# Kernel optimization log

Hardware: AMD Instinct MI355X
Metric: run time of the kernel (lower is better)

## Reference

```python
import jax, jax.numpy as jnp
import numpy as np

N_NODES = 50000
N_EDGES = 800000
HIDDEN = 128
N_GRAPHS = 64


def _linear_init(key, fan_in, shape):
    # torch.nn.Linear default init: U(-1/sqrt(fan_in), 1/sqrt(fan_in))
    bound = 1.0 / np.sqrt(fan_in)
    return jax.random.uniform(key, shape, jnp.float32, -bound, bound)


def setup_inputs() -> dict:
    key = jax.random.key(0)
    ks = jax.random.split(key, 13)
    x = jax.random.normal(ks[0], (N_NODES, HIDDEN), jnp.float32)
    edge_index = jax.random.randint(ks[1], (2, N_EDGES), 0, N_NODES, dtype=jnp.int64)
    batch = jnp.sort(jax.random.randint(ks[2], (N_NODES,), 0, N_GRAPHS, dtype=jnp.int64))
    H = HIDDEN
    return {
        "x": x,
        "edge_index": edge_index,
        "batch": batch,
        "W1a": _linear_init(ks[3], H, (H, H)),
        "b1a": _linear_init(ks[4], H, (H,)),
        "W2a": _linear_init(ks[5], H, (H, H)),
        "b2a": _linear_init(ks[6], H, (H,)),
        "W1b": _linear_init(ks[7], H, (H, H)),
        "b1b": _linear_init(ks[8], H, (H,)),
        "W2b": _linear_init(ks[9], H, (H, H)),
        "b2b": _linear_init(ks[10], H, (H,)),
        "Wfc": _linear_init(ks[11], H, (H, 1)),
        "bfc": _linear_init(ks[12], H, (1,)),
    }


def _gin_conv(x, src, dst, W1, b1, W2, b2):
    # GINConv with eps=0: mlp((1+eps)*x + sum_{j->i} x_j)
    agg = jax.ops.segment_sum(x[src], dst, num_segments=N_NODES) + x
    h = jax.nn.gelu(agg @ W1 + b1, approximate=False)  # exact erf GELU (torch default)
    return jax.nn.gelu(h @ W2 + b2, approximate=False)


def reference(x, edge_index, batch, W1a, b1a, W2a, b2a, W1b, b1b, W2b, b2b, Wfc, bfc):
    src, dst = edge_index[0], edge_index[1]  # messages flow src -> dst (PyG convention)
    h = _gin_conv(x, src, dst, W1a, b1a, W2a, b2a)
    h = _gin_conv(h, src, dst, W1b, b1b, W2b, b2b)
    y = h @ Wfc + bfc  # [N, 1]
    return jax.ops.segment_sum(y, batch, num_segments=N_GRAPHS)  # [G, 1]
```

## Files before the change

### kernel.cpp

```cpp
#include <hip/hip_runtime.h>
#include <hip/hip_bf16.h>
#include <math.h>

#define N_NODES 50000
#define N_EDGES 800000
#define HID 128
#define N_GRAPHS 64
#define BCAP 64

#define ELOOP 8
#define EB ((N_EDGES + 256 * ELOOP - 1) / (256 * ELOOP))
#define RANGES 8
#define RSPAN ((N_NODES + RANGES - 1) / RANGES)
#define CONV_B 782
#define PREP_B 256
#define PREP_GRID (EB * RANGES + CONV_B + PREP_B)

typedef __bf16 bfv8 __attribute__((ext_vector_type(8)));
typedef float f32x4 __attribute__((ext_vector_type(4)));

__device__ __forceinline__ unsigned short f2bf(float f) {
    unsigned int u = __float_as_uint(f);
    u += 0x7fff + ((u >> 16) & 1);
    return (unsigned short)(u >> 16);
}
__device__ __forceinline__ float bflo(unsigned int u) { return __uint_as_float(u << 16); }
__device__ __forceinline__ float bfhi(unsigned int u) { return __uint_as_float(u & 0xffff0000u); }

__device__ __forceinline__ float gelu_f(float x) {
    float x3 = x * x * x;
    float z = 1.5957691216f * x + 0.0713548162f * x3;
    float e = __expf(z);
    float t = 1.f - 2.f / (e + 1.f);
    return 0.5f * x * (1.f + t);
}

__global__ __launch_bounds__(256) void prep_all(
    const int* __restrict__ src, const int* __restrict__ dst,
    int* __restrict__ counts, unsigned short* __restrict__ bucket,
    const float4* __restrict__ xin, ushort4* __restrict__ xb4,
    const float* __restrict__ W1a, const float* __restrict__ W2a,
    const float* __restrict__ W1b, const float* __restrict__ W2b,
    unsigned short* __restrict__ Wt) {
    int b = blockIdx.x;
    int t = threadIdx.x;
    if (b < EB * RANGES) {
        int r = b % RANGES;
        int chunk = b / RANGES;
        int lo = r * RSPAN;
        int hi = min(lo + RSPAN, N_NODES);
        int e0 = chunk * (256 * ELOOP) + t;
        #pragma unroll
        for (int j = 0; j < ELOOP; ++j) {
            int e = e0 + j * 256;
            if (e < N_EDGES) {
                int d = dst[e];
                if (d >= lo && d < hi) {
                    int pos = atomicAdd(&counts[d], 1);
                    if (pos < BCAP) bucket[(size_t)d * BCAP + pos] = (unsigned short)src[e];
                }
            }
        }
    } else if (b < EB * RANGES + CONV_B) {
        int bc = b - EB * RANGES;
        const int n4 = N_NODES * HID / 4;
        #pragma unroll
        for (int j = 0; j < 8; ++j) {
            int i = bc * 2048 + j * 256 + t;
            if (i < n4) {
                float4 v = xin[i];
                ushort4 o;
                o.x = f2bf(v.x); o.y = f2bf(v.y); o.z = f2bf(v.z); o.w = f2bf(v.w);
                xb4[i] = o;
            }
        }
    } else {
        int i = (b - EB * RANGES - CONV_B) * 256 + t;
        int m = i >> 14;
        int rr = (i >> 7) & 127;
        int cc = i & 127;
        const float* W = (m == 0) ? W1a : (m == 1) ? W2a : (m == 2) ? W1b : W2b;
        Wt[i] = f2bf(W[cc * HID + rr]);
    }
}

__global__ __launch_bounds__(256) void aggregate8(const unsigned short* __restrict__ xb,
                                                  const int* __restrict__ counts,
                                                  const unsigned short* __restrict__ bucket,
                                                  unsigned short* __restrict__ agg) {
    int node = blockIdx.x * 4 + (threadIdx.x >> 6);
    if (node >= N_NODES) return;
    int lane = threadIdx.x & 63;
    int g = lane >> 3;
    int c = lane & 7;
    int cnt = min(counts[node], BCAP);
    int eidx = (int)bucket[(size_t)node * BCAP + lane];
    float a[16];
    #pragma unroll
    for (int j = 0; j < 16; ++j) a[j] = 0.f;
    int kmax = (cnt + 7) >> 3;
    #pragma unroll 2
    for (int k = 0; k < kmax; ++k) {
        int i = 8 * k + g;
        int s = __shfl(eidx, (i < cnt) ? i : 0);
        if (i < cnt) {
            const unsigned short* row = xb + (size_t)s * HID + c * 16;
            uint4 u0 = *(const uint4*)(row);
            uint4 u1 = *(const uint4*)(row + 8);
            a[0] += bflo(u0.x); a[1] += bfhi(u0.x);
            a[2] += bflo(u0.y); a[3] += bfhi(u0.y);
            a[4] += bflo(u0.z); a[5] += bfhi(u0.z);
            a[6] += bflo(u0.w); a[7] += bfhi(u0.w);
            a[8] += bflo(u1.x); a[9] += bfhi(u1.x);
            a[10] += bflo(u1.y); a[11] += bfhi(u1.y);
            a[12] += bflo(u1.z); a[13] += bfhi(u1.z);
            a[14] += bflo(u1.w); a[15] += bfhi(u1.w);
        }
    }
    #pragma unroll
    for (int j = 0; j < 16; ++j) {
        a[j] += __shfl_xor(a[j], 8);
        a[j] += __shfl_xor(a[j], 16);
        a[j] += __shfl_xor(a[j], 32);
    }
    if (g == 0) {
        const unsigned short* row = xb + (size_t)node * HID + c * 16;
        uint4 u0 = *(const uint4*)(row);
        uint4 u1 = *(const uint4*)(row + 8);
        a[0] += bflo(u0.x); a[1] += bfhi(u0.x);
        a[2] += bflo(u0.y); a[3] += bfhi(u0.y);
        a[4] += bflo(u0.z); a[5] += bfhi(u0.z);
        a[6] += bflo(u0.w); a[7] += bfhi(u0.w);
        a[8] += bflo(u1.x); a[9] += bfhi(u1.x);
        a[10] += bflo(u1.y); a[11] += bfhi(u1.y);
        a[12] += bflo(u1.z); a[13] += bfhi(u1.z);
        a[14] += bflo(u1.w); a[15] += bfhi(u1.w);
        uint4 o0, o1;
        o0.x = (unsigned int)f2bf(a[0]) | ((unsigned int)f2bf(a[1]) << 16);
        o0.y = (unsigned int)f2bf(a[2]) | ((unsigned int)f2bf(a[3]) << 16);
        o0.z = (unsigned int)f2bf(a[4]) | ((unsigned int)f2bf(a[5]) << 16);
        o0.w = (unsigned int)f2bf(a[6]) | ((unsigned int)f2bf(a[7]) << 16);
        o1.x = (unsigned int)f2bf(a[8]) | ((unsigned int)f2bf(a[9]) << 16);
        o1.y = (unsigned int)f2bf(a[10]) | ((unsigned int)f2bf(a[11]) << 16);
        o1.z = (unsigned int)f2bf(a[12]) | ((unsigned int)f2bf(a[13]) << 16);
        o1.w = (unsigned int)f2bf(a[14]) | ((unsigned int)f2bf(a[15]) << 16);
        unsigned short* orow = agg + (size_t)node * HID + c * 16;
        *(uint4*)(orow) = o0;
        *(uint4*)(orow + 8) = o1;
    }
}

#define LDP 136
__global__ __launch_bounds__(512) void mlp_fused(const unsigned short* __restrict__ A,
                                                 const unsigned short* __restrict__ Wt1,
                                                 const float* __restrict__ b1,
                                                 const unsigned short* __restrict__ Wt2,
                                                 const float* __restrict__ b2,
                                                 unsigned short* __restrict__ out, int nrows) {
    __shared__ __align__(16) unsigned short sA[128][LDP];
    __shared__ __align__(16) unsigned short sT[128][LDP];
    const int t = threadIdx.x;
    const int row0 = blockIdx.x * 128;

    #pragma unroll
    for (int rr = 0; rr < 4; ++rr) {
        int idx = t + rr * 512;
        int r = idx >> 4;
        int cb = (idx & 15) * 8;
        int gr = row0 + r;
        ulonglong2 v = {0ull, 0ull};
        if (gr < nrows) v = *(const ulonglong2*)(A + (size_t)gr * HID + cb);
        *(ulonglong2*)(&sA[r][cb]) = v;
    }

    const int w = t >> 6;
    const int l = t & 63;
    const int lr = l & 15;
    const int lkg = l >> 4;
    const int lk = lkg * 8;
    const int cw = w * 16 + lr;

    bfv8 w1f[4], w2f[4];
    #pragma unroll
    for (int kc = 0; kc < 4; ++kc) {
        w1f[kc] = *(const bfv8*)(Wt1 + (size_t)cw * HID + kc * 32 + lk);
        w2f[kc] = *(const bfv8*)(Wt2 + (size_t)cw * HID + kc * 32 + lk);
    }
    float bias1 = b1[cw];
    float bias2 = b2[cw];
    __syncthreads();

    f32x4 acc[8];
    #pragma unroll
    for (int m = 0; m < 8; ++m) acc[m] = (f32x4){0.f, 0.f, 0.f, 0.f};
    #pragma unroll
    for (int m = 0; m < 8; ++m) {
        #pragma unroll
        for (int kc = 0; kc < 4; ++kc) {
            bfv8 af = *(const bfv8*)(&sA[m * 16 + lr][kc * 32 + lk]);
            acc[m] = __builtin_amdgcn_mfma_f32_16x16x32_bf16(af, w1f[kc], acc[m], 0, 0, 0);
        }
    }
    #pragma unroll
    for (int m = 0; m < 8; ++m) {
        #pragma unroll
        for (int i = 0; i < 4; ++i) {
            float v = gelu_f(acc[m][i] + bias1);
            sT[m * 16 + lkg * 4 + i][cw] = f2bf(v);
        }
    }
    __syncthreads();

    #pragma unroll
    for (int m = 0; m < 8; ++m) acc[m] = (f32x4){0.f, 0.f, 0.f, 0.f};
    #pragma unroll
    for (int m = 0; m < 8; ++m) {
        #pragma unroll
        for (int kc = 0; kc < 4; ++kc) {
            bfv8 af = *(const bfv8*)(&sT[m * 16 + lr][kc * 32 + lk]);
            acc[m] = __builtin_amdgcn_mfma_f32_16x16x32_bf16(af, w2f[kc], acc[m], 0, 0, 0);
        }
    }
    #pragma unroll
    for (int m = 0; m < 8; ++m) {
        #pragma unroll
        for (int i = 0; i < 4; ++i) {
            float v = gelu_f(acc[m][i] + bias2);
            sA[m * 16 + lkg * 4 + i][cw] = f2bf(v);
        }
    }
    __syncthreads();
    #pragma unroll
    for (int rr = 0; rr < 4; ++rr) {
        int idx = t + rr * 512;
        int r = idx >> 4;
        int cb = (idx & 15) * 8;
        int gr = row0 + r;
        if (gr < nrows)
            *(ulonglong2*)(out + (size_t)gr * HID + cb) = *(const ulonglong2*)(&sA[r][cb]);
    }
}

__global__ __launch_bounds__(512) void mlp_final(const unsigned short* __restrict__ A,
                                                 const unsigned short* __restrict__ Wt1,
                                                 const float* __restrict__ b1,
                                                 const unsigned short* __restrict__ Wt2,
                                                 const float* __restrict__ b2,
                                                 const float* __restrict__ Wfc,
                                                 const float* __restrict__ bfc,
                                                 const int* __restrict__ batch,
                                                 float* __restrict__ out, int nrows) {
    __shared__ __align__(16) unsigned short sA[128][LDP];
    __shared__ __align__(16) unsigned short sT[128][LDP];
    __shared__ float bins[N_GRAPHS];
    const int t = threadIdx.x;
    const int row0 = blockIdx.x * 128;
    if (t < N_GRAPHS) bins[t] = 0.f;

    #pragma unroll
    for (int rr = 0; rr < 4; ++rr) {
        int idx = t + rr * 512;
        int r = idx >> 4;
        int cb = (idx & 15) * 8;
        int gr = row0 + r;
        ulonglong2 v = {0ull, 0ull};
        if (gr < nrows) v = *(const ulonglong2*)(A + (size_t)gr * HID + cb);
        *(ulonglong2*)(&sA[r][cb]) = v;
    }

    const int w = t >> 6;
    const int l = t & 63;
    const int lr = l & 15;
    const int lkg = l >> 4;
    const int lk = lkg * 8;
    const int cw = w * 16 + lr;

    bfv8 w1f[4], w2f[4];
    #pragma unroll
    for (int kc = 0; kc < 4; ++kc) {
        w1f[kc] = *(const bfv8*)(Wt1 + (size_t)cw * HID + kc * 32 + lk);
        w2f[kc] = *(const bfv8*)(Wt2 + (size_t)cw * HID + kc * 32 + lk);
    }
    float bias1 = b1[cw];
    float bias2 = b2[cw];
    __syncthreads();

    f32x4 acc[8];
    #pragma unroll
    for (int m = 0; m < 8; ++m) acc[m] = (f32x4){0.f, 0.f, 0.f, 0.f};
    #pragma unroll
    for (int m = 0; m < 8; ++m) {
        #pragma unroll
        for (int kc = 0; kc < 4; ++kc) {
            bfv8 af = *(const bfv8*)(&sA[m * 16 + lr][kc * 32 + lk]);
            acc[m] = __builtin_amdgcn_mfma_f32_16x16x32_bf16(af, w1f[kc], acc[m], 0, 0, 0);
        }
    }
    #pragma unroll
    for (int m = 0; m < 8; ++m) {
        #pragma unroll
        for (int i = 0; i < 4; ++i) {
            float v = gelu_f(acc[m][i] + bias1);
            sT[m * 16 + lkg * 4 + i][cw] = f2bf(v);
        }
    }
    __syncthreads();

    #pragma unroll
    for (int m = 0; m < 8; ++m) acc[m] = (f32x4){0.f, 0.f, 0.f, 0.f};
    #pragma unroll
    for (int m = 0; m < 8; ++m) {
        #pragma unroll
        for (int kc = 0; kc < 4; ++kc) {
            bfv8 af = *(const bfv8*)(&sT[m * 16 + lr][kc * 32 + lk]);
            acc[m] = __builtin_amdgcn_mfma_f32_16x16x32_bf16(af, w2f[kc], acc[m], 0, 0, 0);
        }
    }
    #pragma unroll
    for (int m = 0; m < 8; ++m) {
        #pragma unroll
        for (int i = 0; i < 4; ++i) {
            float v = gelu_f(acc[m][i] + bias2);
            sA[m * 16 + lkg * 4 + i][cw] = f2bf(v);
        }
    }
    __syncthreads();

    {
        int row = w * 16 + (l >> 2);
        int q = l & 3;
        int gr = row0 + row;
        float acc2 = 0.f;
        if (gr < nrows) {
            const uint4* hrow = (const uint4*)(&sA[row][q * 32]);
            #pragma unroll
            for (int jj = 0; jj < 4; ++jj) {
                uint4 v = hrow[jj];
                int f = q * 32 + jj * 8;
                acc2 += bflo(v.x) * Wfc[f]     + bfhi(v.x) * Wfc[f + 1];
                acc2 += bflo(v.y) * Wfc[f + 2] + bfhi(v.y) * Wfc[f + 3];
                acc2 += bflo(v.z) * Wfc[f + 4] + bfhi(v.z) * Wfc[f + 5];
                acc2 += bflo(v.w) * Wfc[f + 6] + bfhi(v.w) * Wfc[f + 7];
            }
        }
        acc2 += __shfl_xor(acc2, 1);
        acc2 += __shfl_xor(acc2, 2);
        if (q == 0 && gr < nrows) atomicAdd(&bins[batch[gr]], acc2 + bfc[0]);
    }
    __syncthreads();
    if (t < N_GRAPHS && bins[t] != 0.f) atomicAdd(&out[t], bins[t]);
}

extern "C" void kernel_launch(void* const* d_in, const int* in_sizes, int n_in,
                              void* d_out, int out_size, void* d_ws, size_t ws_size,
                              hipStream_t stream) {
    const float* x    = (const float*)d_in[0];
    const int*   ei   = (const int*)d_in[1];
    const int*   bat  = (const int*)d_in[2];
    const float* W1a  = (const float*)d_in[3];
    const float* b1a  = (const float*)d_in[4];
    const float* W2a  = (const float*)d_in[5];
    const float* b2a  = (const float*)d_in[6];
    const float* W1b  = (const float*)d_in[7];
    const float* b1b  = (const float*)d_in[8];
    const float* W2b  = (const float*)d_in[9];
    const float* b2b  = (const float*)d_in[10];
    const float* Wfc  = (const float*)d_in[11];
    const float* bfc  = (const float*)d_in[12];
    float* out = (float*)d_out;

    const int* src = ei;
    const int* dst = ei + N_EDGES;

    unsigned short* xb     = (unsigned short*)d_ws;
    unsigned short* bufA   = xb + (size_t)N_NODES * HID;
    unsigned short* bufB   = bufA + (size_t)N_NODES * HID;
    unsigned short* Wt     = bufB + (size_t)N_NODES * HID;
    int* counts = (int*)(Wt + 4 * HID * HID);
    unsigned short* bucket = (unsigned short*)(counts + N_NODES);

    hipMemsetAsync(out, 0, N_GRAPHS * sizeof(float), stream);
    hipMemsetAsync(counts, 0, N_NODES * sizeof(int), stream);

    prep_all<<<PREP_GRID, 256, 0, stream>>>(src, dst, counts, bucket,
                                            (const float4*)x, (ushort4*)xb,
                                            W1a, W2a, W1b, W2b, Wt);

    const int agg_blocks = (N_NODES + 3) / 4;
    const int mlp_blocks = (N_NODES + 127) / 128;
    unsigned short* Wt1a = Wt;
    unsigned short* Wt2a = Wt + HID * HID;
    unsigned short* Wt1b = Wt + 2 * HID * HID;
    unsigned short* Wt2b = Wt + 3 * HID * HID;

    aggregate8<<<agg_blocks, 256, 0, stream>>>(xb, counts, bucket, bufA);
    mlp_fused<<<mlp_blocks, 512, 0, stream>>>(bufA, Wt1a, b1a, Wt2a, b2a, bufB, N_NODES);

    aggregate8<<<agg_blocks, 256, 0, stream>>>(bufB, counts, bucket, bufA);
    mlp_final<<<mlp_blocks, 512, 0, stream>>>(bufA, Wt1b, b1b, Wt2b, b2b,
                                              Wfc, bfc, bat, out, N_NODES);
}
```

Before: 240.0 us.

## Pad edge counters, process two nodes per wave, halve MLP row tile

Edge bucketing drops the eight-way destination-range replication: each edge is now visited once, and its per-node counter is padded to a 64-byte stride to reduce atomic contention on shared cache lines. The aggregation kernel now has each wavefront handle two nodes, interleaving their gathers to expose more memory-level parallelism. Both MLP kernels move from 128-row to 64-row tiles, doubling the block count and halving shared memory per block. The costs are a 16x larger counter array to memset, more registers in the aggregation kernel, and weight fragments reloaded per block twice as often.

```diff
diff --git a/kernel.cpp b/kernel.cpp
--- a/kernel.cpp
+++ b/kernel.cpp
@@ -7,14 +7,13 @@
 #define HID 128
 #define N_GRAPHS 64
 #define BCAP 64
+#define CSTR 16
 
 #define ELOOP 8
 #define EB ((N_EDGES + 256 * ELOOP - 1) / (256 * ELOOP))
-#define RANGES 8
-#define RSPAN ((N_NODES + RANGES - 1) / RANGES)
 #define CONV_B 782
 #define PREP_B 256
-#define PREP_GRID (EB * RANGES + CONV_B + PREP_B)
+#define PREP_GRID (EB + CONV_B + PREP_B)
 
 typedef __bf16 bfv8 __attribute__((ext_vector_type(8)));
 typedef float f32x4 __attribute__((ext_vector_type(4)));
@@ -44,25 +43,19 @@
     unsigned short* __restrict__ Wt) {
     int b = blockIdx.x;
     int t = threadIdx.x;
-    if (b < EB * RANGES) {
-        int r = b % RANGES;
-        int chunk = b / RANGES;
-        int lo = r * RSPAN;
-        int hi = min(lo + RSPAN, N_NODES);
-        int e0 = chunk * (256 * ELOOP) + t;
+    if (b < EB) {
+        int e0 = b * (256 * ELOOP) + t;
         #pragma unroll
         for (int j = 0; j < ELOOP; ++j) {
             int e = e0 + j * 256;
             if (e < N_EDGES) {
                 int d = dst[e];
-                if (d >= lo && d < hi) {
-                    int pos = atomicAdd(&counts[d], 1);
-                    if (pos < BCAP) bucket[(size_t)d * BCAP + pos] = (unsigned short)src[e];
-                }
+                int pos = atomicAdd(&counts[d * CSTR], 1);
+                if (pos < BCAP) bucket[(size_t)d * BCAP + pos] = (unsigned short)src[e];
             }
         }
-    } else if (b < EB * RANGES + CONV_B) {
-        int bc = b - EB * RANGES;
+    } else if (b < EB + CONV_B) {
+        int bc = b - EB;
         const int n4 = N_NODES * HID / 4;
         #pragma unroll
         for (int j = 0; j < 8; ++j) {
@@ -75,7 +68,7 @@
             }
         }
     } else {
-        int i = (b - EB * RANGES - CONV_B) * 256 + t;
+        int i = (b - EB - CONV_B) * 256 + t;
         int m = i >> 14;
         int rr = (i >> 7) & 127;
         int cc = i & 127;
@@ -88,65 +81,113 @@
                                                   const int* __restrict__ counts,
                                                   const unsigned short* __restrict__ bucket,
                                                   unsigned short* __restrict__ agg) {
-    int node = blockIdx.x * 4 + (threadIdx.x >> 6);
-    if (node >= N_NODES) return;
-    int lane = threadIdx.x & 63;
-    int g = lane >> 3;
-    int c = lane & 7;
-    int cnt = min(counts[node], BCAP);
-    int eidx = (int)bucket[(size_t)node * BCAP + lane];
-    float a[16];
-    #pragma unroll
-    for (int j = 0; j < 16; ++j) a[j] = 0.f;
-    int kmax = (cnt + 7) >> 3;
-    #pragma unroll 2
-    for (int k = 0; k < kmax; ++k) {
+    int wid = threadIdx.x >> 6;
+    int node0 = blockIdx.x * 8 + wid * 2;
+    int node1 = node0 + 1;
+    bool v0 = node0 < N_NODES, v1 = node1 < N_NODES;
+    if (!v0) return;
+    int l = threadIdx.x & 63;
+    int g = l >> 3;
+    int c = l & 7;
+    int cnt0 = min(counts[node0 * CSTR], BCAP);
+    int cnt1 = v1 ? min(counts[node1 * CSTR], BCAP) : 0;
+    int e0 = (int)bucket[(size_t)node0 * BCAP + l];
+    int e1 = v1 ? (int)bucket[(size_t)node1 * BCAP + l] : 0;
+    float a0[16], a1[16];
+    #pragma unroll
+    for (int j = 0; j < 16; ++j) { a0[j] = 0.f; a1[j] = 0.f; }
+    int km = max((cnt0 + 7) >> 3, (cnt1 + 7) >> 3);
+    for (int k = 0; k < km; ++k) {
         int i = 8 * k + g;
-        int s = __shfl(eidx, (i < cnt) ? i : 0);
-        if (i < cnt) {
-            const unsigned short* row = xb + (size_t)s * HID + c * 16;
+        int s0 = __shfl(e0, (i < cnt0) ? i : 0);
+        int s1 = __shfl(e1, (i < cnt1) ? i : 0);
+        if (i < cnt0) {
+            const unsigned short* row = xb + (size_t)s0 * HID + c * 16;
             uint4 u0 = *(const uint4*)(row);
             uint4 u1 = *(const uint4*)(row + 8);
-            a[0] += bflo(u0.x); a[1] += bfhi(u0.x);
-            a[2] += bflo(u0.y); a[3] += bfhi(u0.y);
-            a[4] += bflo(u0.z); a[5] += bfhi(u0.z);
-            a[6] += bflo(u0.w); a[7] += bfhi(u0.w);
-            a[8] += bflo(u1.x); a[9] += bfhi(u1.x);
-            a[10] += bflo(u1.y); a[11] += bfhi(u1.y);
-            a[12] += bflo(u1.z); a[13] += bfhi(u1.z);
-            a[14] += bflo(u1.w); a[15] += bfhi(u1.w);
+            a0[0] += bflo(u0.x); a0[1] += bfhi(u0.x);
+            a0[2] += bflo(u0.y); a0[3] += bfhi(u0.y);
+            a0[4] += bflo(u0.z); a0[5] += bfhi(u0.z);
+            a0[6] += bflo(u0.w); a0[7] += bfhi(u0.w);
+            a0[8] += bflo(u1.x); a0[9] += bfhi(u1.x);
+            a0[10] += bflo(u1.y); a0[11] += bfhi(u1.y);
+            a0[12] += bflo(u1.z); a0[13] += bfhi(u1.z);
+            a0[14] += bflo(u1.w); a0[15] += bfhi(u1.w);
+        }
+        if (i < cnt1) {
+            const unsigned short* row = xb + (size_t)s1 * HID + c * 16;
+            uint4 u0 = *(const uint4*)(row);
+            uint4 u1 = *(const uint4*)(row + 8);
+            a1[0] += bflo(u0.x); a1[1] += bfhi(u0.x);
+            a1[2] += bflo(u0.y); a1[3] += bfhi(u0.y);
+            a1[4] += bflo(u0.z); a1[5] += bfhi(u0.z);
+            a1[6] += bflo(u0.w); a1[7] += bfhi(u0.w);
+            a1[8] += bflo(u1.x); a1[9] += bfhi(u1.x);
+            a1[10] += bflo(u1.y); a1[11] += bfhi(u1.y);
+            a1[12] += bflo(u1.z); a1[13] += bfhi(u1.z);
+            a1[14] += bflo(u1.w); a1[15] += bfhi(u1.w);
         }
     }
     #pragma unroll
     for (int j = 0; j < 16; ++j) {
-        a[j] += __shfl_xor(a[j], 8);
-        a[j] += __shfl_xor(a[j], 16);
-        a[j] += __shfl_xor(a[j], 32);
+        a0[j] += __shfl_xor(a0[j], 8);
+        a0[j] += __shfl_xor(a0[j], 16);
+        a0[j] += __shfl_xor(a0[j], 32);
+        a1[j] += __shfl_xor(a1[j], 8);
+        a1[j] += __shfl_xor(a1[j], 16);
+        a1[j] += __shfl_xor(a1[j], 32);
     }
     if (g == 0) {
-        const unsigned short* row = xb + (size_t)node * HID + c * 16;
-        uint4 u0 = *(const uint4*)(row);
-        uint4 u1 = *(const uint4*)(row + 8);
-        a[0] += bflo(u0.x); a[1] += bfhi(u0.x);
-        a[2] += bflo(u0.y); a[3] += bfhi(u0.y);
-        a[4] += bflo(u0.z); a[5] += bfhi(u0.z);
-        a[6] += bflo(u0.w); a[7] += bfhi(u0.w);
-        a[8] += bflo(u1.x); a[9] += bfhi(u1.x);
-        a[10] += bflo(u1.y); a[11] += bfhi(u1.y);
-        a[12] += bflo(u1.z); a[13] += bfhi(u1.z);
-        a[14] += bflo(u1.w); a[15] += bfhi(u1.w);
-        uint4 o0, o1;
-        o0.x = (unsigned int)f2bf(a[0]) | ((unsigned int)f2bf(a[1]) << 16);
-        o0.y = (unsigned int)f2bf(a[2]) | ((unsigned int)f2bf(a[3]) << 16);
-        o0.z = (unsigned int)f2bf(a[4]) | ((unsigned int)f2bf(a[5]) << 16);
-        o0.w = (unsigned int)f2bf(a[6]) | ((unsigned int)f2bf(a[7]) << 16);
-        o1.x = (unsigned int)f2bf(a[8]) | ((unsigned int)f2bf(a[9]) << 16);
-        o1.y = (unsigned int)f2bf(a[10]) | ((unsigned int)f2bf(a[11]) << 16);
-        o1.z = (unsigned int)f2bf(a[12]) | ((unsigned int)f2bf(a[13]) << 16);
-        o1.w = (unsigned int)f2bf(a[14]) | ((unsigned int)f2bf(a[15]) << 16);
-        unsigned short* orow = agg + (size_t)node * HID + c * 16;
-        *(uint4*)(orow) = o0;
-        *(uint4*)(orow + 8) = o1;
+        {
+            const unsigned short* row = xb + (size_t)node0 * HID + c * 16;
+            uint4 u0 = *(const uint4*)(row);
+            uint4 u1 = *(const uint4*)(row + 8);
+            a0[0] += bflo(u0.x); a0[1] += bfhi(u0.x);
+            a0[2] += bflo(u0.y); a0[3] += bfhi(u0.y);
+            a0[4] += bflo(u0.z); a0[5] += bfhi(u0.z);
+            a0[6] += bflo(u0.w); a0[7] += bfhi(u0.w);
+            a0[8] += bflo(u1.x); a0[9] += bfhi(u1.x);
+            a0[10] += bflo(u1.y); a0[11] += bfhi(u1.y);
+            a0[12] += bflo(u1.z); a0[13] += bfhi(u1.z);
+            a0[14] += bflo(u1.w); a0[15] += bfhi(u1.w);
+            uint4 o0, o1;
+            o0.x = (unsigned int)f2bf(a0[0]) | ((unsigned int)f2bf(a0[1]) << 16);
+            o0.y = (unsigned int)f2bf(a0[2]) | ((unsigned int)f2bf(a0[3]) << 16);
+            o0.z = (unsigned int)f2bf(a0[4]) | ((unsigned int)f2bf(a0[5]) << 16);
+            o0.w = (unsigned int)f2bf(a0[6]) | ((unsigned int)f2bf(a0[7]) << 16);
+            o1.x = (unsigned int)f2bf(a0[8]) | ((unsigned int)f2bf(a0[9]) << 16);
+            o1.y = (unsigned int)f2bf(a0[10]) | ((unsigned int)f2bf(a0[11]) << 16);
+            o1.z = (unsigned int)f2bf(a0[12]) | ((unsigned int)f2bf(a0[13]) << 16);
+            o1.w = (unsigned int)f2bf(a0[14]) | ((unsigned int)f2bf(a0[15]) << 16);
+            unsigned short* orow = agg + (size_t)node0 * HID + c * 16;
+            *(uint4*)(orow) = o0;
+            *(uint4*)(orow + 8) = o1;
+        }
+        if (v1) {
+            const unsigned short* row = xb + (size_t)node1 * HID + c * 16;
+            uint4 u0 = *(const uint4*)(row);
+            uint4 u1 = *(const uint4*)(row + 8);
+            a1[0] += bflo(u0.x); a1[1] += bfhi(u0.x);
+            a1[2] += bflo(u0.y); a1[3] += bfhi(u0.y);
+            a1[4] += bflo(u0.z); a1[5] += bfhi(u0.z);
+            a1[6] += bflo(u0.w); a1[7] += bfhi(u0.w);
+            a1[8] += bflo(u1.x); a1[9] += bfhi(u1.x);
+            a1[10] += bflo(u1.y); a1[11] += bfhi(u1.y);
+            a1[12] += bflo(u1.z); a1[13] += bfhi(u1.z);
+            a1[14] += bflo(u1.w); a1[15] += bfhi(u1.w);
+            uint4 o0, o1;
+            o0.x = (unsigned int)f2bf(a1[0]) | ((unsigned int)f2bf(a1[1]) << 16);
+            o0.y = (unsigned int)f2bf(a1[2]) | ((unsigned int)f2bf(a1[3]) << 16);
+            o0.z = (unsigned int)f2bf(a1[4]) | ((unsigned int)f2bf(a1[5]) << 16);
+            o0.w = (unsigned int)f2bf(a1[6]) | ((unsigned int)f2bf(a1[7]) << 16);
+            o1.x = (unsigned int)f2bf(a1[8]) | ((unsigned int)f2bf(a1[9]) << 16);
+            o1.y = (unsigned int)f2bf(a1[10]) | ((unsigned int)f2bf(a1[11]) << 16);
+            o1.z = (unsigned int)f2bf(a1[12]) | ((unsigned int)f2bf(a1[13]) << 16);
+            o1.w = (unsigned int)f2bf(a1[14]) | ((unsigned int)f2bf(a1[15]) << 16);
+            unsigned short* orow = agg + (size_t)node1 * HID + c * 16;
+            *(uint4*)(orow) = o0;
+            *(uint4*)(orow + 8) = o1;
+        }
     }
 }
 
@@ -157,13 +198,13 @@
                                                  const unsigned short* __restrict__ Wt2,
                                                  const float* __restrict__ b2,
                                                  unsigned short* __restrict__ out, int nrows) {
-    __shared__ __align__(16) unsigned short sA[128][LDP];
-    __shared__ __align__(16) unsigned short sT[128][LDP];
+    __shared__ __align__(16) unsigned short sA[64][LDP];
+    __shared__ __align__(16) unsigned short sT[64][LDP];
     const int t = threadIdx.x;
-    const int row0 = blockIdx.x * 128;
-
-    #pragma unroll
-    for (int rr = 0; rr < 4; ++rr) {
+    const int row0 = blockIdx.x * 64;
+
+    #pragma unroll
+    for (int rr = 0; rr < 2; ++rr) {
         int idx = t + rr * 512;
         int r = idx >> 4;
         int cb = (idx & 15) * 8;
@@ -190,11 +231,11 @@
     float bias2 = b2[cw];
     __syncthreads();
 
-    f32x4 acc[8];
-    #pragma unroll
-    for (int m = 0; m < 8; ++m) acc[m] = (f32x4){0.f, 0.f, 0.f, 0.f};
-    #pragma unroll
-    for (int m = 0; m < 8; ++m) {
+    f32x4 acc[4];
+    #pragma unroll
+    for (int m = 0; m < 4; ++m) acc[m] = (f32x4){0.f, 0.f, 0.f, 0.f};
+    #pragma unroll
+    for (int m = 0; m < 4; ++m) {
         #pragma unroll
         for (int kc = 0; kc < 4; ++kc) {
             bfv8 af = *(const bfv8*)(&sA[m * 16 + lr][kc * 32 + lk]);
@@ -202,7 +243,7 @@
         }
     }
     #pragma unroll
-    for (int m = 0; m < 8; ++m) {
+    for (int m = 0; m < 4; ++m) {
         #pragma unroll
         for (int i = 0; i < 4; ++i) {
             float v = gelu_f(acc[m][i] + bias1);
@@ -212,9 +253,9 @@
     __syncthreads();
 
     #pragma unroll
-    for (int m = 0; m < 8; ++m) acc[m] = (f32x4){0.f, 0.f, 0.f, 0.f};
-    #pragma unroll
-    for (int m = 0; m < 8; ++m) {
+    for (int m = 0; m < 4; ++m) acc[m] = (f32x4){0.f, 0.f, 0.f, 0.f};
+    #pragma unroll
+    for (int m = 0; m < 4; ++m) {
         #pragma unroll
         for (int kc = 0; kc < 4; ++kc) {
             bfv8 af = *(const bfv8*)(&sT[m * 16 + lr][kc * 32 + lk]);
@@ -222,7 +263,7 @@
         }
     }
     #pragma unroll
-    for (int m = 0; m < 8; ++m) {
+    for (int m = 0; m < 4; ++m) {
         #pragma unroll
         for (int i = 0; i < 4; ++i) {
             float v = gelu_f(acc[m][i] + bias2);
@@ -231,7 +272,7 @@
     }
     __syncthreads();
     #pragma unroll
-    for (int rr = 0; rr < 4; ++rr) {
+    for (int rr = 0; rr < 2; ++rr) {
         int idx = t + rr * 512;
         int r = idx >> 4;
         int cb = (idx & 15) * 8;
@@ -250,15 +291,15 @@
                                                  const float* __restrict__ bfc,
                                                  const int* __restrict__ batch,
                                                  float* __restrict__ out, int nrows) {
-    __shared__ __align__(16) unsigned short sA[128][LDP];
-    __shared__ __align__(16) unsigned short sT[128][LDP];
+    __shared__ __align__(16) unsigned short sA[64][LDP];
+    __shared__ __align__(16) unsigned short sT[64][LDP];
     __shared__ float bins[N_GRAPHS];
     const int t = threadIdx.x;
-    const int row0 = blockIdx.x * 128;
+    const int row0 = blockIdx.x * 64;
     if (t < N_GRAPHS) bins[t] = 0.f;
 
     #pragma unroll
-    for (int rr = 0; rr < 4; ++rr) {
+    for (int rr = 0; rr < 2; ++rr) {
         int idx = t + rr * 512;
         int r = idx >> 4;
         int cb = (idx & 15) * 8;
@@ -285,11 +326,11 @@
     float bias2 = b2[cw];
     __syncthreads();
 
-    f32x4 acc[8];
-    #pragma unroll
-    for (int m = 0; m < 8; ++m) acc[m] = (f32x4){0.f, 0.f, 0.f, 0.f};
-    #pragma unroll
-    for (int m = 0; m < 8; ++m) {
+    f32x4 acc[4];
+    #pragma unroll
+    for (int m = 0; m < 4; ++m) acc[m] = (f32x4){0.f, 0.f, 0.f, 0.f};
+    #pragma unroll
+    for (int m = 0; m < 4; ++m) {
         #pragma unroll
         for (int kc = 0; kc < 4; ++kc) {
             bfv8 af = *(const bfv8*)(&sA[m * 16 + lr][kc * 32 + lk]);
@@ -297,7 +338,7 @@
         }
     }
     #pragma unroll
-    for (int m = 0; m < 8; ++m) {
+    for (int m = 0; m < 4; ++m) {
         #pragma unroll
         for (int i = 0; i < 4; ++i) {
             float v = gelu_f(acc[m][i] + bias1);
@@ -307,9 +348,9 @@
     __syncthreads();
 
     #pragma unroll
-    for (int m = 0; m < 8; ++m) acc[m] = (f32x4){0.f, 0.f, 0.f, 0.f};
-    #pragma unroll
-    for (int m = 0; m < 8; ++m) {
+    for (int m = 0; m < 4; ++m) acc[m] = (f32x4){0.f, 0.f, 0.f, 0.f};
+    #pragma unroll
+    for (int m = 0; m < 4; ++m) {
         #pragma unroll
         for (int kc = 0; kc < 4; ++kc) {
             bfv8 af = *(const bfv8*)(&sT[m * 16 + lr][kc * 32 + lk]);
@@ -317,7 +358,7 @@
         }
     }
     #pragma unroll
-    for (int m = 0; m < 8; ++m) {
+    for (int m = 0; m < 4; ++m) {
         #pragma unroll
         for (int i = 0; i < 4; ++i) {
             float v = gelu_f(acc[m][i] + bias2);
@@ -327,16 +368,16 @@
     __syncthreads();
 
     {
-        int row = w * 16 + (l >> 2);
-        int q = l & 3;
+        int row = t >> 3;
+        int q = t & 7;
         int gr = row0 + row;
         float acc2 = 0.f;
         if (gr < nrows) {
-            const uint4* hrow = (const uint4*)(&sA[row][q * 32]);
+            const uint4* hrow = (const uint4*)(&sA[row][q * 16]);
             #pragma unroll
-            for (int jj = 0; jj < 4; ++jj) {
+            for (int jj = 0; jj < 2; ++jj) {
                 uint4 v = hrow[jj];
-                int f = q * 32 + jj * 8;
+                int f = q * 16 + jj * 8;
                 acc2 += bflo(v.x) * Wfc[f]     + bfhi(v.x) * Wfc[f + 1];
                 acc2 += bflo(v.y) * Wfc[f + 2] + bfhi(v.y) * Wfc[f + 3];
                 acc2 += bflo(v.z) * Wfc[f + 4] + bfhi(v.z) * Wfc[f + 5];
@@ -345,6 +386,7 @@
         }
         acc2 += __shfl_xor(acc2, 1);
         acc2 += __shfl_xor(acc2, 2);
+        acc2 += __shfl_xor(acc2, 4);
         if (q == 0 && gr < nrows) atomicAdd(&bins[batch[gr]], acc2 + bfc[0]);
     }
     __syncthreads();
@@ -377,17 +419,17 @@
     unsigned short* bufB   = bufA + (size_t)N_NODES * HID;
     unsigned short* Wt     = bufB + (size_t)N_NODES * HID;
     int* counts = (int*)(Wt + 4 * HID * HID);
-    unsigned short* bucket = (unsigned short*)(counts + N_NODES);
+    unsigned short* bucket = (unsigned short*)(counts + (size_t)N_NODES * CSTR);
 
     hipMemsetAsync(out, 0, N_GRAPHS * sizeof(float), stream);
-    hipMemsetAsync(counts, 0, N_NODES * sizeof(int), stream);
+    hipMemsetAsync(counts, 0, (size_t)N_NODES * CSTR * sizeof(int), stream);
 
     prep_all<<<PREP_GRID, 256, 0, stream>>>(src, dst, counts, bucket,
                                             (const float4*)x, (ushort4*)xb,
                                             W1a, W2a, W1b, W2b, Wt);
 
-    const int agg_blocks = (N_NODES + 3) / 4;
-    const int mlp_blocks = (N_NODES + 127) / 128;
+    const int agg_blocks = (N_NODES + 7) / 8;
+    const int mlp_blocks = (N_NODES + 63) / 64;
     unsigned short* Wt1a = Wt;
     unsigned short* Wt2a = Wt + HID * HID;
     unsigned short* Wt1b = Wt + 2 * HID * HID;
```

Result: slower. 252.1 us (+5.1%).
